# Performance work log

Hardware: AMD Instinct MI355X
Metric: run time of the kernel (lower is better)

Reference implementation:

```python
import jax, jax.numpy as jnp
import numpy as np

L_F, HOP, DELTA, L_S, COND, GH = 32, 16, 3, 96, 32, 64
B, T = 128, 48000


def setup_inputs() -> dict:
    key = jax.random.key(0)
    ks = jax.random.split(key, 12)
    s = 0.05
    return {
        "x": jax.random.normal(ks[0], (B, T), jnp.float32),
        # GRU (PyTorch layout): weight_ih (3H, L_S), weight_hh (3H, H)
        "W_ih": jax.random.normal(ks[1], (3 * GH, L_S), jnp.float32) * s,
        "W_hh": jax.random.normal(ks[2], (3 * GH, GH), jnp.float32) * s,
        "b_ih": jax.random.normal(ks[3], (3 * GH,), jnp.float32) * s,
        "b_hh": jax.random.normal(ks[4], (3 * GH,), jnp.float32) * s,
        # SlowBranch output projection -> cond_dim
        "W_cs": jax.random.normal(ks[5], (COND, GH), jnp.float32) * s,
        "b_cs": jax.random.normal(ks[6], (COND,), jnp.float32) * s,
        # FastEC MLP
        "W1": jax.random.normal(ks[7], (GH, L_F + COND), jnp.float32) * s,
        "b1": jax.random.normal(ks[8], (GH,), jnp.float32) * s,
        "W2": jax.random.normal(ks[9], (L_F, GH), jnp.float32) * s,
        "b2": jax.random.normal(ks[10], (L_F,), jnp.float32) * s,
    }


def reference(x, W_ih, W_hh, b_ih, b_hh, W_cs, b_cs, W1, b1, W2, b2):
    Bsz, Tlen = x.shape
    Nf = (Tlen - L_F) // HOP + 1
    win_s = DELTA * HOP * 2
    hop_s = DELTA * HOP
    Ns = (Tlen - win_s) // hop_s + 1

    f_starts = jnp.arange(Nf) * HOP                      # (Nf,)
    fast_idx = f_starts[:, None] + jnp.arange(L_F)       # (Nf, L_F)
    fast_frames = x[:, fast_idx]                         # (B, Nf, L_F)

    s_starts = jnp.arange(Ns) * hop_s
    slow_frames = x[:, s_starts[:, None] + jnp.arange(win_s)]  # (B, Ns, L_S)

    # Single-layer GRU over slow frames (PyTorch gate order r, z, n)
    def step(h, xt):
        gi = xt @ W_ih.T + b_ih                          # (B, 3H)
        gh = h @ W_hh.T + b_hh
        i_r, i_z, i_n = jnp.split(gi, 3, axis=-1)
        h_r, h_z, h_n = jnp.split(gh, 3, axis=-1)
        r = jax.nn.sigmoid(i_r + h_r)
        z = jax.nn.sigmoid(i_z + h_z)
        n = jnp.tanh(i_n + r * h_n)
        hn = (1.0 - z) * n + z * h
        return hn, hn

    h0 = jnp.zeros((Bsz, GH), x.dtype)
    _, hs = jax.lax.scan(step, h0, jnp.swapaxes(slow_frames, 0, 1))
    hs = jnp.swapaxes(hs, 0, 1)                          # (B, Ns, GH)
    c_s = hs @ W_cs.T + b_cs                             # (B, Ns, COND)

    # per-fast-frame conditioning vector (gather)
    idx = jnp.clip(jnp.arange(Nf) // DELTA - 1, 0, None)
    c = c_s[:, idx]                                      # (B, Nf, COND)

    # FastEC batched over all frames at once
    h = jnp.concatenate([fast_frames, c], axis=-1)       # (B, Nf, L_F+COND)
    h = jax.nn.relu(h @ W1.T + b1)
    y = h @ W2.T + b2                                    # (B, Nf, L_F)

    # overlap-add scatter
    out = jnp.zeros_like(x).at[:, fast_idx].add(y)
    return out
```

## Files before the change

kernel.cpp:

```cpp
#include <hip/hip_runtime.h>

constexpr int Bn  = 128;
constexpr int Tn  = 48000;
constexpr int NFn = 2999;
constexpr int NSn = 999;
constexpr int G3n = 192;
constexpr int GHn = 64;

typedef float f2 __attribute__((ext_vector_type(2)));
typedef float f4 __attribute__((ext_vector_type(4)));

__global__ __launch_bounds__(192) void gi_kernel(const float* __restrict__ x,
                                                 const float* __restrict__ W_ih,
                                                 const float* __restrict__ b_ih,
                                                 float* __restrict__ GI) {
  __shared__ __align__(16) float WT[48 * 196];
  __shared__ float xs[1584];
  const int tile = blockIdx.x;
  const int b    = blockIdx.y;
  const int t0   = tile * 32;
  const int nt   = min(32, NSn - t0);
  const int tid  = threadIdx.x;

  const int span = (nt - 1) * 48 + 96;
  for (int i = tid; i < 1584; i += 192)
    xs[i] = (i < span) ? x[(size_t)b * Tn + t0 * 48 + i] : 0.0f;

  const int jq = tid % 48;
  const int tg = tid / 48;
  const int j0 = jq * 4;

  float acc[8][4];
#pragma unroll
  for (int u = 0; u < 8; ++u)
#pragma unroll
    for (int jj = 0; jj < 4; ++jj) acc[u][jj] = b_ih[j0 + jj];

  for (int half = 0; half < 2; ++half) {
    __syncthreads();
    for (int e = tid; e < 192 * 48; e += 192) {
      int j = e / 48, k = e % 48;
      WT[k * 196 + j] = W_ih[j * 96 + half * 48 + k];
    }
    __syncthreads();
    for (int k = 0; k < 48; ++k) {
      float4 w = *(const float4*)&WT[k * 196 + j0];
#pragma unroll
      for (int u = 0; u < 8; ++u) {
        float xv = xs[(tg * 8 + u) * 48 + half * 48 + k];
        acc[u][0] = fmaf(xv, w.x, acc[u][0]);
        acc[u][1] = fmaf(xv, w.y, acc[u][1]);
        acc[u][2] = fmaf(xv, w.z, acc[u][2]);
        acc[u][3] = fmaf(xv, w.w, acc[u][3]);
      }
    }
  }

#pragma unroll
  for (int u = 0; u < 8; ++u) {
    int tl = tg * 8 + u;
    if (tl < nt) {
      float4 st = make_float4(acc[u][0], acc[u][1], acc[u][2], acc[u][3]);
      *(float4*)&GI[(size_t)(b * NSn + t0 + tl) * G3n + j0] = st;
    }
  }
}

__device__ __forceinline__ float fsigmoid(float v) {
  return __fdividef(1.0f, 1.0f + __expf(-v));
}
__device__ __forceinline__ float ftanh_f(float v) {
  return 1.0f - __fdividef(2.0f, __expf(2.0f * v) + 1.0f);
}

__device__ __forceinline__ void gru_body(const float* __restrict__ GI,
                                         const float* __restrict__ W_hh,
                                         const float* __restrict__ b_hh,
                                         float* __restrict__ hs,
                                         float* hbuf, int b, int j) {
  f2 wr2[32], wz2[32], wn2[32];
  const f2* Wr = (const f2*)(W_hh + (size_t)j * 64);
  const f2* Wz = (const f2*)(W_hh + (size_t)(j + 64) * 64);
  const f2* Wn = (const f2*)(W_hh + (size_t)(j + 128) * 64);
#pragma unroll
  for (int q = 0; q < 32; ++q) { wr2[q] = Wr[q]; wz2[q] = Wz[q]; wn2[q] = Wn[q]; }
#pragma unroll
  for (int q = 0; q < 32; ++q) {
    asm volatile("" : "+v"(wr2[q]));
    asm volatile("" : "+v"(wz2[q]));
    asm volatile("" : "+v"(wn2[q]));
  }
  const float br = b_hh[j], bz = b_hh[j + 64], bn = b_hh[j + 128];

  hbuf[j] = 0.0f;
  float hj = 0.0f;
  __builtin_amdgcn_wave_barrier();

  const float* gp = GI + (size_t)b * NSn * G3n;
  float* hsp = hs + (size_t)b * NSn * GHn;

  float pr0, pr1, pr2, pz0, pz1, pz2, pn0, pn1, pn2;
  pr0 = gp[0 * G3n + j];       pz0 = gp[0 * G3n + 64 + j];  pn0 = gp[0 * G3n + 128 + j];
  pr1 = gp[1 * G3n + j];       pz1 = gp[1 * G3n + 64 + j];  pn1 = gp[1 * G3n + 128 + j];

  for (int t = 0; t < NSn; ++t) {
    const size_t off = (size_t)min(t + 2, NSn - 1) * G3n;
    pr2 = gp[off + j];
    pz2 = gp[off + 64 + j];
    pn2 = gp[off + 128 + j];

    const f2* h2 = (const f2*)hbuf;
    f2 ar0 = {0.f, 0.f}, ar1 = {0.f, 0.f}, ar2 = {0.f, 0.f}, ar3 = {0.f, 0.f};
    f2 az0 = {0.f, 0.f}, az1 = {0.f, 0.f}, az2 = {0.f, 0.f}, az3 = {0.f, 0.f};
    f2 an0 = {0.f, 0.f}, an1 = {0.f, 0.f}, an2 = {0.f, 0.f}, an3 = {0.f, 0.f};
#pragma unroll
    for (int q = 0; q < 8; ++q) {
      f2 h0 = h2[q * 4 + 0], h1 = h2[q * 4 + 1], h2v = h2[q * 4 + 2], h3 = h2[q * 4 + 3];
      ar0 += wr2[q * 4 + 0] * h0; ar1 += wr2[q * 4 + 1] * h1;
      ar2 += wr2[q * 4 + 2] * h2v; ar3 += wr2[q * 4 + 3] * h3;
      az0 += wz2[q * 4 + 0] * h0; az1 += wz2[q * 4 + 1] * h1;
      az2 += wz2[q * 4 + 2] * h2v; az3 += wz2[q * 4 + 3] * h3;
      an0 += wn2[q * 4 + 0] * h0; an1 += wn2[q * 4 + 1] * h1;
      an2 += wn2[q * 4 + 2] * h2v; an3 += wn2[q * 4 + 3] * h3;
    }
    f2 sr = (ar0 + ar1) + (ar2 + ar3);
    f2 sz = (az0 + az1) + (az2 + az3);
    f2 sn = (an0 + an1) + (an2 + an3);

    float r = fsigmoid(pr0 + br + sr.x + sr.y);
    float z = fsigmoid(pz0 + bz + sz.x + sz.y);
    float n = ftanh_f(fmaf(r, bn + sn.x + sn.y, pn0));
    float hn = fmaf(z, hj - n, n);

    __builtin_amdgcn_wave_barrier();
    hbuf[j] = hn;
    __builtin_amdgcn_wave_barrier();
    hj = hn;
    hsp[(size_t)t * GHn + j] = hn;

    pr0 = pr1; pr1 = pr2;
    pz0 = pz1; pz1 = pz2;
    pn0 = pn1; pn1 = pn2;
  }
}

__global__ __attribute__((amdgpu_flat_work_group_size(64, 64),
                          amdgpu_waves_per_eu(1, 1),
                          amdgpu_num_vgpr(256)))
void gru_kernel(const float* __restrict__ GI,
                const float* __restrict__ W_hh,
                const float* __restrict__ b_hh,
                float* __restrict__ hs) {
  __shared__ __align__(16) float hbuf[64];
  gru_body(GI, W_hh, b_hh, hs, hbuf, blockIdx.x, threadIdx.x);
}

constexpr int UCHUNK = 125;
constexpr int NCH    = 24;

__global__ __attribute__((amdgpu_flat_work_group_size(64, 64),
                          amdgpu_waves_per_eu(1, 1),
                          amdgpu_num_vgpr(256)))
void fat_kernel(const float* __restrict__ GI,
                const float* __restrict__ W_hh,
                const float* __restrict__ b_hh,
                float* __restrict__ hs,
                const float* __restrict__ x,
                const float* __restrict__ W1,
                const float* __restrict__ b1,
                float* __restrict__ U) {
  __shared__ __align__(16) float hbuf[64];
  __shared__ __align__(16) float xs[UCHUNK * 16 + 16];
  const int tid = threadIdx.x;

  if (blockIdx.x < Bn) {
    gru_body(GI, W_hh, b_hh, hs, hbuf, blockIdx.x, tid);
    return;
  }

  const int ub = blockIdx.x - Bn;
  const int b  = ub / NCH;
  const int ch = ub % NCH;
  const int fA = ch * UCHUNK;
  const int fE = min(fA + UCHUNK, NFn);
  const int o  = tid;

  const int nsamp = (fE - fA - 1) * 16 + 32;
  for (int i = tid; i < nsamp; i += 64)
    xs[i] = x[(size_t)b * Tn + fA * 16 + i];

  f4 w1f[8];
#pragma unroll
  for (int i = 0; i < 8; ++i)
    w1f[i] = *(const f4*)&W1[(size_t)o * 64 + 4 * i];
  const float bo = b1[o];
  __syncthreads();

  float* Up = U + ((size_t)b * NFn) * GHn + o;
  for (int f = fA; f < fE; ++f) {
    const f4* xq = (const f4*)&xs[(f - fA) * 16];
    float a0 = bo, a1 = 0.f, a2 = 0.f, a3 = 0.f;
#pragma unroll
    for (int i = 0; i < 8; ++i) {
      f4 xv = xq[i];
      a0 = fmaf(xv[0], w1f[i][0], a0);
      a1 = fmaf(xv[1], w1f[i][1], a1);
      a2 = fmaf(xv[2], w1f[i][2], a2);
      a3 = fmaf(xv[3], w1f[i][3], a3);
    }
    Up[(size_t)f * GHn] = (a0 + a1) + (a2 + a3);
  }
}

__global__ __launch_bounds__(256) void d_kernel(const float* __restrict__ hs,
                                                const float* __restrict__ W_cs,
                                                const float* __restrict__ b_cs,
                                                const float* __restrict__ W1,
                                                float* __restrict__ d) {
  __shared__ __align__(16) float WcT[64 * 36];
  __shared__ __align__(16) float W1cT[32 * 68];
  __shared__ __align__(16) float hsl[32 * 65];
  __shared__ __align__(16) float cloc[32 * 36];
  __shared__ __align__(16) float bcs[32];
  const int tile = blockIdx.x;
  const int b    = blockIdx.y;
  const int t0   = tile * 32;
  const int nt   = min(32, NSn - t0);
  const int tid  = threadIdx.x;

  for (int e = tid; e < 32 * 64; e += 256) {
    int i = e >> 6, k = e & 63;
    WcT[k * 36 + i] = W_cs[e];
  }
  for (int e = tid; e < 64 * 32; e += 256) {
    int o = e >> 5, i = e & 31;
    W1cT[i * 68 + o] = W1[(size_t)o * 64 + 32 + i];
  }
  for (int e = tid; e < nt * 64; e += 256) {
    int t = e >> 6, k = e & 63;
    hsl[t * 65 + k] = hs[((size_t)b * NSn + t0 + t) * GHn + k];
  }
  if (tid < 32) bcs[tid] = b_cs[tid];
  __syncthreads();

  {
    const int iq = tid & 7;
    const int t  = tid >> 3;
    if (t < nt) {
      float4 acc = *(const float4*)&bcs[iq * 4];
      const float* hr = &hsl[t * 65];
#pragma unroll 4
      for (int k = 0; k < 64; ++k) {
        float hv = hr[k];
        float4 w = *(const float4*)&WcT[k * 36 + iq * 4];
        acc.x = fmaf(w.x, hv, acc.x);
        acc.y = fmaf(w.y, hv, acc.y);
        acc.z = fmaf(w.z, hv, acc.z);
        acc.w = fmaf(w.w, hv, acc.w);
      }
      *(float4*)&cloc[t * 36 + iq * 4] = acc;
    }
  }
  __syncthreads();

  for (int it = tid; it < 32 * 16; it += 256) {
    const int oq = it & 15;
    const int t  = it >> 4;
    if (t < nt) {
      float a0 = 0.f, a1 = 0.f, a2 = 0.f, a3 = 0.f;
      const float* cr = &cloc[t * 36];
#pragma unroll 4
      for (int i = 0; i < 32; ++i) {
        float cv = cr[i];
        float4 w = *(const float4*)&W1cT[i * 68 + oq * 4];
        a0 = fmaf(w.x, cv, a0);
        a1 = fmaf(w.y, cv, a1);
        a2 = fmaf(w.z, cv, a2);
        a3 = fmaf(w.w, cv, a3);
      }
      float4 st = make_float4(a0, a1, a2, a3);
      *(float4*)&d[((size_t)b * NSn + t0 + t) * GHn + oq * 4] = st;
    }
  }
}

__global__ __launch_bounds__(256) void cs_kernel(const float* __restrict__ hs,
                                                 const float* __restrict__ W_cs,
                                                 const float* __restrict__ b_cs,
                                                 float* __restrict__ cs) {
  __shared__ __align__(16) float WcT[64 * 36];
  __shared__ __align__(16) float hsl[32 * 65];
  __shared__ __align__(16) float bcs[32];
  const int tile = blockIdx.x;
  const int b    = blockIdx.y;
  const int t0   = tile * 32;
  const int nt   = min(32, NSn - t0);
  const int tid  = threadIdx.x;

  for (int e = tid; e < 32 * 64; e += 256) {
    int i = e >> 6, k = e & 63;
    WcT[k * 36 + i] = W_cs[e];
  }
  for (int e = tid; e < nt * 64; e += 256) {
    int t = e >> 6, k = e & 63;
    hsl[t * 65 + k] = hs[((size_t)b * NSn + t0 + t) * GHn + k];
  }
  if (tid < 32) bcs[tid] = b_cs[tid];
  __syncthreads();

  const int oq = tid & 7;
  const int t  = tid >> 3;
  if (t < nt) {
    float4 acc = *(const float4*)&bcs[oq * 4];
    const float* hr = &hsl[t * 65];
#pragma unroll 4
    for (int k = 0; k < 64; ++k) {
      float hv = hr[k];
      float4 w = *(const float4*)&WcT[k * 36 + oq * 4];
      acc.x = fmaf(w.x, hv, acc.x);
      acc.y = fmaf(w.y, hv, acc.y);
      acc.z = fmaf(w.z, hv, acc.z);
      acc.w = fmaf(w.w, hv, acc.w);
    }
    *(float4*)&cs[((size_t)b * NSn + t0 + t) * 32 + oq * 4] = acc;
  }
}

__global__ __launch_bounds__(256) void out2_kernel(const float* __restrict__ U,
                                                   const float* __restrict__ d,
                                                   const float* __restrict__ W2,
                                                   const float* __restrict__ b2,
                                                   float* __restrict__ out) {
  __shared__ __align__(16) float h1loc[33 * 68];
  __shared__ __align__(16) float W2T[64 * 36];
  __shared__ __align__(16) float yloc[33 * 32];
  __shared__ __align__(16) float dloc[12][68];
  __shared__ __align__(16) float bb2[32];

  const int fb  = blockIdx.x;
  const int b   = blockIdx.y;
  const int f0  = fb * 32;
  const int nf  = min(33, NFn - f0);
  const int tid = threadIdx.x;
  const int ts0 = max(f0 / 3 - 1, 0);

  for (int e = tid; e < 32 * 64; e += 256) {
    int o = e >> 6, k = e & 63;
    W2T[k * 36 + o] = W2[e];
  }
  if (tid < 32) bb2[tid] = b2[tid];
  for (int e = tid; e < 12 * 64; e += 256) {
    int ti = e >> 6, o = e & 63;
    int ts = min(ts0 + ti, NSn - 1);
    dloc[ti][o] = d[((size_t)b * NSn + ts) * GHn + o];
  }
  __syncthreads();

  for (int it = tid; it < 33 * 16; it += 256) {
    const int lf = it >> 4, oq = it & 15;
    const int f  = f0 + lf;
    f4 s = {0.f, 0.f, 0.f, 0.f};
    if (f < NFn) {
      f4 u  = *(const f4*)&U[((size_t)b * NFn + f) * GHn + oq * 4];
      const int ti = max(f / 3 - 1, 0) - ts0;
      f4 dv = *(const f4*)&dloc[ti][oq * 4];
      s = u + dv;
#pragma unroll
      for (int c = 0; c < 4; ++c) s[c] = fmaxf(s[c], 0.f);
    }
    *(f4*)&h1loc[lf * 68 + oq * 4] = s;
  }
  __syncthreads();

  for (int it = tid; it < 33 * 8; it += 256) {
    const int lf = it >> 3, oq = it & 7;
    float4 acc = *(const float4*)&bb2[oq * 4];
    const float* hr = &h1loc[lf * 68];
#pragma unroll 4
    for (int k = 0; k < 64; ++k) {
      float hv = hr[k];
      float4 w = *(const float4*)&W2T[k * 36 + oq * 4];
      acc.x = fmaf(w.x, hv, acc.x);
      acc.y = fmaf(w.y, hv, acc.y);
      acc.z = fmaf(w.z, hv, acc.z);
      acc.w = fmaf(w.w, hv, acc.w);
    }
    *(float4*)&yloc[lf * 32 + oq * 4] = acc;
  }
  __syncthreads();

  const int s0 = f0 * 16 + 16;
  const int s1 = min(s0 + 512, Tn);
  for (int s = s0 + tid; s < s1; s += 256) {
    int f1  = s >> 4;
    int o1  = s & 15;
    int lf1 = f1 - f0;
    float v = yloc[(lf1 - 1) * 32 + o1 + 16];
    if (lf1 < nf) v += yloc[lf1 * 32 + o1];
    out[(size_t)b * Tn + s] = v;
  }
  if (fb == 0 && tid < 16) out[(size_t)b * Tn + tid] = yloc[tid];
}

__global__ __launch_bounds__(256) void out_kernel(const float* __restrict__ x,
                                                  const float* __restrict__ cs,
                                                  const float* __restrict__ W1,
                                                  const float* __restrict__ b1,
                                                  const float* __restrict__ W2,
                                                  const float* __restrict__ b2,
                                                  float* __restrict__ out) {
  __shared__ __align__(16) float A[33 * 65];
  __shared__ __align__(16) float W1T[64 * 68];
  __shared__ __align__(16) float W2T[64 * 36];
  __shared__ __align__(16) float h1loc[33 * 65];
  __shared__ __align__(16) float yloc[33 * 32];
  __shared__ __align__(16) float bb1[64];
  __shared__ __align__(16) float bb2[32];

  const int fb  = blockIdx.x;
  const int b   = blockIdx.y;
  const int f0  = fb * 32;
  const int nf  = min(33, NFn - f0);
  const int tid = threadIdx.x;

  for (int e = tid; e < 64 * 64; e += 256) {
    int o = e >> 6, k = e & 63;
    W1T[k * 68 + o] = W1[e];
  }
  for (int e = tid; e < 32 * 64; e += 256) {
    int o = e >> 6, k = e & 63;
    W2T[k * 36 + o] = W2[e];
  }
  if (tid < 64) bb1[tid] = b1[tid];
  if (tid < 32) bb2[tid] = b2[tid];

  for (int e = tid; e < 33 * 32; e += 256) {
    int lf = e >> 5, k = e & 31;
    int g = (f0 + lf) * 16 + k;
    A[lf * 65 + k] = (lf < nf && g < Tn) ? x[(size_t)b * Tn + g] : 0.0f;
  }
  for (int e = tid; e < 33 * 32; e += 256) {
    int lf = e >> 5, k = e & 31;
    int ts = max((f0 + lf) / 3 - 1, 0);
    A[lf * 65 + 32 + k] = (lf < nf) ? cs[((size_t)b * NSn + ts) * 32 + k] : 0.0f;
  }
  __syncthreads();

  for (int it = tid; it < 33 * 16; it += 256) {
    int lf = it >> 4, oq = it & 15;
    float4 acc = *(const float4*)&bb1[oq * 4];
    const float* ar = &A[lf * 65];
#pragma unroll 4
    for (int k = 0; k < 64; ++k) {
      float av = ar[k];
      float4 w = *(const float4*)&W1T[k * 68 + oq * 4];
      acc.x = fmaf(w.x, av, acc.x);
      acc.y = fmaf(w.y, av, acc.y);
      acc.z = fmaf(w.z, av, acc.z);
      acc.w = fmaf(w.w, av, acc.w);
    }
    acc.x = fmaxf(acc.x, 0.0f); acc.y = fmaxf(acc.y, 0.0f);
    acc.z = fmaxf(acc.z, 0.0f); acc.w = fmaxf(acc.w, 0.0f);
    *(float4*)&h1loc[lf * 65 + oq * 4] = acc;
  }
  __syncthreads();

  for (int it = tid; it < 33 * 8; it += 256) {
    int lf = it >> 3, oq = it & 7;
    float4 acc = *(const float4*)&bb2[oq * 4];
    const float* hr = &h1loc[lf * 65];
#pragma unroll 4
    for (int k = 0; k < 64; ++k) {
      float hv = hr[k];
      float4 w = *(const float4*)&W2T[k * 36 + oq * 4];
      acc.x = fmaf(w.x, hv, acc.x);
      acc.y = fmaf(w.y, hv, acc.y);
      acc.z = fmaf(w.z, hv, acc.z);
      acc.w = fmaf(w.w, hv, acc.w);
    }
    *(float4*)&yloc[lf * 32 + oq * 4] = acc;
  }
  __syncthreads();

  const int s0 = f0 * 16 + 16;
  const int s1 = min(s0 + 512, Tn);
  for (int s = s0 + tid; s < s1; s += 256) {
    int f1  = s >> 4;
    int o1  = s & 15;
    int lf1 = f1 - f0;
    float v = yloc[(lf1 - 1) * 32 + o1 + 16];
    if (lf1 < nf) v += yloc[lf1 * 32 + o1];
    out[(size_t)b * Tn + s] = v;
  }
  if (fb == 0 && tid < 16) out[(size_t)b * Tn + tid] = yloc[tid];
}

extern "C" void kernel_launch(void* const* d_in, const int* in_sizes, int n_in,
                              void* d_out, int out_size, void* d_ws, size_t ws_size,
                              hipStream_t stream) {
  const float* x    = (const float*)d_in[0];
  const float* W_ih = (const float*)d_in[1];
  const float* W_hh = (const float*)d_in[2];
  const float* b_ih = (const float*)d_in[3];
  const float* b_hh = (const float*)d_in[4];
  const float* W_cs = (const float*)d_in[5];
  const float* b_cs = (const float*)d_in[6];
  const float* W1   = (const float*)d_in[7];
  const float* b1   = (const float*)d_in[8];
  const float* W2   = (const float*)d_in[9];
  const float* b2   = (const float*)d_in[10];
  float* out = (float*)d_out;

  const size_t giN = (size_t)Bn * NSn * G3n;
  const size_t hsN = (size_t)Bn * NSn * GHn;
  const size_t uN  = (size_t)Bn * NFn * GHn;

  float* GI = (float*)d_ws;
  float* hs = GI + giN;

  gi_kernel<<<dim3(32, Bn), 192, 0, stream>>>(x, W_ih, b_ih, GI);

  if (ws_size >= (giN + hsN + uN) * sizeof(float)) {
    float* U = hs + hsN;
    float* d = GI;
    fat_kernel<<<Bn + Bn * NCH, 64, 0, stream>>>(GI, W_hh, b_hh, hs,
                                                 x, W1, b1, U);
    d_kernel<<<dim3(32, Bn), 256, 0, stream>>>(hs, W_cs, b_cs, W1, d);
    out2_kernel<<<dim3(94, Bn), 256, 0, stream>>>(U, d, W2, b2, out);
  } else {
    float* cs = GI;
    gru_kernel<<<Bn, 64, 0, stream>>>(GI, W_hh, b_hh, hs);
    cs_kernel<<<dim3(32, Bn), 256, 0, stream>>>(hs, W_cs, b_cs, cs);
    out_kernel<<<dim3(94, Bn), 256, 0, stream>>>(x, cs, W1, b1, W2, b2, out);
  }
}
```

Before: 771.6 us.

## Fuse GI projection and GRU into a cooperative kernel with per-chunk flags

Replaces the separate GI-projection kernel and the fat kernel with one cooperative mega kernel. Worker blocks compute GI tiles in time-chunk order and publish per-(batch, chunk) readiness counters. The GRU blocks spin on those flags and start the recurrence before all of GI is ready, so the sequential GRU overlaps with the projection and the U computation. The flags live in the output buffer, which later kernels overwrite. It relies on 1024 co-resident blocks, a grid sync, and spin-waiting with memory fences.

After: 1.344 ms. 1.74x slower.

```diff
diff --git a/kernel.cpp b/kernel.cpp
--- a/kernel.cpp
+++ b/kernel.cpp
@@ -1,4 +1,7 @@
 #include <hip/hip_runtime.h>
+#include <hip/hip_cooperative_groups.h>
+
+namespace cg = cooperative_groups;
 
 constexpr int Bn  = 128;
 constexpr int Tn  = 48000;
@@ -73,11 +76,13 @@
   return 1.0f - __fdividef(2.0f, __expf(2.0f * v) + 1.0f);
 }
 
+template <bool POLL>
 __device__ __forceinline__ void gru_body(const float* __restrict__ GI,
                                          const float* __restrict__ W_hh,
                                          const float* __restrict__ b_hh,
                                          float* __restrict__ hs,
-                                         float* hbuf, int b, int j) {
+                                         float* hbuf, int b, int j,
+                                         unsigned int* flags) {
   f2 wr2[32], wz2[32], wn2[32];
   const f2* Wr = (const f2*)(W_hh + (size_t)j * 64);
   const f2* Wz = (const f2*)(W_hh + (size_t)(j + 64) * 64);
@@ -92,6 +97,18 @@
   }
   const float br = b_hh[j], bz = b_hh[j + 64], bn = b_hh[j + 128];
 
+  unsigned int* fl = POLL ? (flags + b * 32) : nullptr;
+  int cur_tc = 0;
+  if (POLL) {
+    if (j == 0) {
+      while (__hip_atomic_load(&fl[0], __ATOMIC_ACQUIRE,
+                               __HIP_MEMORY_SCOPE_AGENT) < 3u)
+        __builtin_amdgcn_s_sleep(4);
+    }
+    __builtin_amdgcn_wave_barrier();
+    __threadfence();
+  }
+
   hbuf[j] = 0.0f;
   float hj = 0.0f;
   __builtin_amdgcn_wave_barrier();
@@ -104,7 +121,21 @@
   pr1 = gp[1 * G3n + j];       pz1 = gp[1 * G3n + 64 + j];  pn1 = gp[1 * G3n + 128 + j];
 
   for (int t = 0; t < NSn; ++t) {
-    const size_t off = (size_t)min(t + 2, NSn - 1) * G3n;
+    const int tn = min(t + 2, NSn - 1);
+    if (POLL) {
+      const int tc2 = tn >> 5;
+      if (tc2 != cur_tc) {
+        if (j == 0) {
+          while (__hip_atomic_load(&fl[tc2], __ATOMIC_ACQUIRE,
+                                   __HIP_MEMORY_SCOPE_AGENT) < 3u)
+            __builtin_amdgcn_s_sleep(4);
+        }
+        __builtin_amdgcn_wave_barrier();
+        __threadfence();
+        cur_tc = tc2;
+      }
+    }
+    const size_t off = (size_t)tn * G3n;
     pr2 = gp[off + j];
     pz2 = gp[off + 64 + j];
     pn2 = gp[off + 128 + j];
@@ -152,7 +183,7 @@
                 const float* __restrict__ b_hh,
                 float* __restrict__ hs) {
   __shared__ __align__(16) float hbuf[64];
-  gru_body(GI, W_hh, b_hh, hs, hbuf, blockIdx.x, threadIdx.x);
+  gru_body<false>(GI, W_hh, b_hh, hs, hbuf, blockIdx.x, threadIdx.x, nullptr);
 }
 
 constexpr int UCHUNK = 125;
@@ -174,7 +205,7 @@
   const int tid = threadIdx.x;
 
   if (blockIdx.x < Bn) {
-    gru_body(GI, W_hh, b_hh, hs, hbuf, blockIdx.x, tid);
+    gru_body<false>(GI, W_hh, b_hh, hs, hbuf, blockIdx.x, tid, nullptr);
     return;
   }
 
@@ -209,6 +240,136 @@
       a3 = fmaf(xv[3], w1f[i][3], a3);
     }
     Up[(size_t)f * GHn] = (a0 + a1) + (a2 + a3);
+  }
+}
+
+constexpr int NWORK  = 896;
+constexpr int NBLK   = 1024;
+constexpr int GTILES = Bn * 32 * 3;
+
+__global__ __attribute__((amdgpu_flat_work_group_size(64, 64),
+                          amdgpu_waves_per_eu(1, 1),
+                          amdgpu_num_vgpr(256)))
+void mega_kernel(float* __restrict__ GI,
+                 const float* __restrict__ W_hh,
+                 const float* __restrict__ b_hh,
+                 float* __restrict__ hs,
+                 const float* __restrict__ x,
+                 const float* __restrict__ W_ih,
+                 const float* __restrict__ b_ih,
+                 const float* __restrict__ W1,
+                 const float* __restrict__ b1,
+                 float* __restrict__ U,
+                 unsigned int* __restrict__ flags) {
+  __shared__ __align__(16) float smem[3168];
+  const int tid = threadIdx.x;
+
+  for (int i = blockIdx.x * 64 + tid; i < Bn * 32; i += NBLK * 64)
+    flags[i] = 0u;
+  __threadfence();
+  cg::this_grid().sync();
+
+  if (blockIdx.x >= NWORK) {
+    gru_body<true>(GI, W_hh, b_hh, hs, smem, blockIdx.x - NWORK, tid, flags);
+    return;
+  }
+
+  float* WQ = smem;
+  float* xs = smem + 1536;
+  const int jq = tid & 15;
+  const int tg = tid >> 4;
+  const int j0 = jq * 4;
+
+  for (int tile = blockIdx.x; tile < GTILES; tile += NWORK) {
+    const int tc = tile / (Bn * 3);
+    const int rr = tile - tc * (Bn * 3);
+    const int b  = rr / 3;
+    const int g  = rr - b * 3;
+    const int nt = min(32, NSn - tc * 32);
+    const int span = (nt - 1) * 48 + 96;
+
+    __builtin_amdgcn_wave_barrier();
+    for (int i = tid; i < 1584; i += 64)
+      xs[i] = (i < span) ? x[(size_t)b * Tn + tc * 1536 + i] : 0.0f;
+
+    float acc[8][4];
+#pragma unroll
+    for (int u = 0; u < 8; ++u)
+#pragma unroll
+      for (int jj = 0; jj < 4; ++jj) acc[u][jj] = b_ih[g * 64 + j0 + jj];
+
+    for (int q = 0; q < 4; ++q) {
+      __builtin_amdgcn_wave_barrier();
+      {
+        const float* src = &W_ih[(size_t)(g * 64 + tid) * 96 + q * 24];
+#pragma unroll
+        for (int i2 = 0; i2 < 6; ++i2) {
+          f4 v = *(const f4*)&src[4 * i2];
+#pragma unroll
+          for (int c = 0; c < 4; ++c) WQ[(i2 * 4 + c) * 64 + tid] = v[c];
+        }
+      }
+      __builtin_amdgcn_wave_barrier();
+      for (int k = 0; k < 24; ++k) {
+        f4 w = *(const f4*)&WQ[k * 64 + j0];
+#pragma unroll
+        for (int u = 0; u < 8; ++u) {
+          float xv = xs[(tg * 8 + u) * 48 + q * 24 + k];
+          acc[u][0] = fmaf(xv, w[0], acc[u][0]);
+          acc[u][1] = fmaf(xv, w[1], acc[u][1]);
+          acc[u][2] = fmaf(xv, w[2], acc[u][2]);
+          acc[u][3] = fmaf(xv, w[3], acc[u][3]);
+        }
+      }
+    }
+
+#pragma unroll
+    for (int u = 0; u < 8; ++u) {
+      int tl = tg * 8 + u;
+      if (tl < nt) {
+        float4 st = make_float4(acc[u][0], acc[u][1], acc[u][2], acc[u][3]);
+        *(float4*)&GI[((size_t)(b * NSn + tc * 32 + tl)) * G3n + g * 64 + j0] = st;
+      }
+    }
+    __threadfence();
+    if (tid == 0)
+      __hip_atomic_fetch_add(&flags[b * 32 + tc], 1u, __ATOMIC_RELEASE,
+                             __HIP_MEMORY_SCOPE_AGENT);
+  }
+
+  float* xu = smem;
+  f4 w1f[8];
+#pragma unroll
+  for (int i = 0; i < 8; ++i)
+    w1f[i] = *(const f4*)&W1[(size_t)tid * 64 + 4 * i];
+  const float bo = b1[tid];
+
+  for (int ut = blockIdx.x; ut < Bn * NCH; ut += NWORK) {
+    const int b  = ut / NCH;
+    const int ch = ut % NCH;
+    const int fA = ch * UCHUNK;
+    const int fE = min(fA + UCHUNK, NFn);
+    const int nsamp = (fE - fA - 1) * 16 + 32;
+
+    __builtin_amdgcn_wave_barrier();
+    for (int i = tid; i < nsamp; i += 64)
+      xu[i] = x[(size_t)b * Tn + fA * 16 + i];
+    __builtin_amdgcn_wave_barrier();
+
+    float* Up = U + ((size_t)b * NFn) * GHn + tid;
+    for (int f = fA; f < fE; ++f) {
+      const f4* xq = (const f4*)&xu[(f - fA) * 16];
+      float a0 = bo, a1 = 0.f, a2 = 0.f, a3 = 0.f;
+#pragma unroll
+      for (int i = 0; i < 8; ++i) {
+        f4 xv = xq[i];
+        a0 = fmaf(xv[0], w1f[i][0], a0);
+        a1 = fmaf(xv[1], w1f[i][1], a1);
+        a2 = fmaf(xv[2], w1f[i][2], a2);
+        a3 = fmaf(xv[3], w1f[i][3], a3);
+      }
+      Up[(size_t)f * GHn] = (a0 + a1) + (a2 + a3);
+    }
   }
 }
 
@@ -518,17 +679,28 @@
   float* GI = (float*)d_ws;
   float* hs = GI + giN;
 
-  gi_kernel<<<dim3(32, Bn), 192, 0, stream>>>(x, W_ih, b_ih, GI);
-
   if (ws_size >= (giN + hsN + uN) * sizeof(float)) {
     float* U = hs + hsN;
     float* d = GI;
-    fat_kernel<<<Bn + Bn * NCH, 64, 0, stream>>>(GI, W_hh, b_hh, hs,
-                                                 x, W1, b1, U);
+    unsigned int* flags = (unsigned int*)out;
+
+    void* args[] = {(void*)&GI, (void*)&W_hh, (void*)&b_hh, (void*)&hs,
+                    (void*)&x,  (void*)&W_ih, (void*)&b_ih, (void*)&W1,
+                    (void*)&b1, (void*)&U,    (void*)&flags};
+    hipError_t e = hipLaunchCooperativeKernel((const void*)mega_kernel,
+                                              dim3(NBLK), dim3(64),
+                                              args, 0, stream);
+    if (e != hipSuccess) {
+      (void)hipGetLastError();
+      gi_kernel<<<dim3(32, Bn), 192, 0, stream>>>(x, W_ih, b_ih, GI);
+      fat_kernel<<<Bn + Bn * NCH, 64, 0, stream>>>(GI, W_hh, b_hh, hs,
+                                                   x, W1, b1, U);
+    }
     d_kernel<<<dim3(32, Bn), 256, 0, stream>>>(hs, W_cs, b_cs, W1, d);
     out2_kernel<<<dim3(94, Bn), 256, 0, stream>>>(U, d, W2, b2, out);
   } else {
     float* cs = GI;
+    gi_kernel<<<dim3(32, Bn), 192, 0, stream>>>(x, W_ih, b_ih, GI);
     gru_kernel<<<Bn, 64, 0, stream>>>(GI, W_hh, b_hh, hs);
     cs_kernel<<<dim3(32, Bn), 256, 0, stream>>>(hs, W_cs, b_cs, cs);
     out_kernel<<<dim3(94, Bn), 256, 0, stream>>>(x, cs, W1, b1, W2, b2, out);
```

## Rewrite GI projection kernel to keep W_ih row in registers per thread

Applied to the files above, without the earlier changes.

Replaces the shared-memory tiled GI kernel with one where each thread holds its full 96-wide W_ih row in registers and streams x frames directly from global memory, two timesteps at a time. Each thread produces one output column across a chunk of 56 slow frames, and the grid shrinks to 18 chunks per batch row. This removes the shared x staging and the transposed weight tile, in exchange for high register pressure (96 weight floats) and redundant broadcast global loads of x across threads. GI is only a small part of the pipeline, so the end-to-end effect is limited.

Result: slower. 870.1 us (+12.8%).

```diff
diff --git a/kernel.cpp b/kernel.cpp
--- a/kernel.cpp
+++ b/kernel.cpp
@@ -10,59 +10,69 @@
 typedef float f2 __attribute__((ext_vector_type(2)));
 typedef float f4 __attribute__((ext_vector_type(4)));
 
-__global__ __launch_bounds__(192) void gi_kernel(const float* __restrict__ x,
-                                                 const float* __restrict__ W_ih,
-                                                 const float* __restrict__ b_ih,
-                                                 float* __restrict__ GI) {
-  __shared__ __align__(16) float WT[48 * 196];
-  __shared__ float xs[1584];
-  const int tile = blockIdx.x;
-  const int b    = blockIdx.y;
-  const int t0   = tile * 32;
-  const int nt   = min(32, NSn - t0);
-  const int tid  = threadIdx.x;
-
-  const int span = (nt - 1) * 48 + 96;
-  for (int i = tid; i < 1584; i += 192)
-    xs[i] = (i < span) ? x[(size_t)b * Tn + t0 * 48 + i] : 0.0f;
-
-  const int jq = tid % 48;
-  const int tg = tid / 48;
-  const int j0 = jq * 4;
-
-  float acc[8][4];
-#pragma unroll
-  for (int u = 0; u < 8; ++u)
-#pragma unroll
-    for (int jj = 0; jj < 4; ++jj) acc[u][jj] = b_ih[j0 + jj];
-
-  for (int half = 0; half < 2; ++half) {
+constexpr int GI_TC = 56;
+constexpr int GI_NC = 18;
+
+__global__ __launch_bounds__(192) void gi2_kernel(const float* __restrict__ x,
+                                                  const float* __restrict__ W_ih,
+                                                  const float* __restrict__ b_ih,
+                                                  float* __restrict__ GI) {
+  __shared__ __align__(16) float WL[192 * 48];
+  const int b  = blockIdx.y;
+  const int t0 = blockIdx.x * GI_TC;
+  const int t1 = min(t0 + GI_TC, NSn);
+  const int j  = threadIdx.x;
+
+  f4 w[24];
+  for (int h = 0; h < 2; ++h) {
     __syncthreads();
-    for (int e = tid; e < 192 * 48; e += 192) {
-      int j = e / 48, k = e % 48;
-      WT[k * 196 + j] = W_ih[j * 96 + half * 48 + k];
+    for (int e = j; e < 192 * 48; e += 192) {
+      const int row = e / 48, kk = e - row * 48;
+      WL[e] = W_ih[row * 96 + h * 48 + kk];
     }
     __syncthreads();
-    for (int k = 0; k < 48; ++k) {
-      float4 w = *(const float4*)&WT[k * 196 + j0];
-#pragma unroll
-      for (int u = 0; u < 8; ++u) {
-        float xv = xs[(tg * 8 + u) * 48 + half * 48 + k];
-        acc[u][0] = fmaf(xv, w.x, acc[u][0]);
-        acc[u][1] = fmaf(xv, w.y, acc[u][1]);
-        acc[u][2] = fmaf(xv, w.z, acc[u][2]);
-        acc[u][3] = fmaf(xv, w.w, acc[u][3]);
-      }
-    }
-  }
-
-#pragma unroll
-  for (int u = 0; u < 8; ++u) {
-    int tl = tg * 8 + u;
-    if (tl < nt) {
-      float4 st = make_float4(acc[u][0], acc[u][1], acc[u][2], acc[u][3]);
-      *(float4*)&GI[(size_t)(b * NSn + t0 + tl) * G3n + j0] = st;
-    }
+#pragma unroll
+    for (int i = 0; i < 12; ++i)
+      w[h * 12 + i] = *(const f4*)&WL[j * 48 + 4 * i];
+  }
+  const float bj = b_ih[j];
+
+  const float* xb = x + (size_t)b * Tn;
+  float* gbase = GI + (size_t)b * NSn * G3n + j;
+
+  int t = t0;
+  for (; t + 2 <= t1; t += 2) {
+    const float* xp0 = xb + t * 48;
+    const float* xp1 = xp0 + 48;
+    float a0 = bj, a1 = bj;
+#pragma unroll
+    for (int q = 0; q < 24; ++q) {
+      f4 x0 = *(const f4*)&xp0[4 * q];
+      f4 x1 = *(const f4*)&xp1[4 * q];
+      a0 = fmaf(x0[0], w[q][0], a0);
+      a0 = fmaf(x0[1], w[q][1], a0);
+      a0 = fmaf(x0[2], w[q][2], a0);
+      a0 = fmaf(x0[3], w[q][3], a0);
+      a1 = fmaf(x1[0], w[q][0], a1);
+      a1 = fmaf(x1[1], w[q][1], a1);
+      a1 = fmaf(x1[2], w[q][2], a1);
+      a1 = fmaf(x1[3], w[q][3], a1);
+    }
+    gbase[(size_t)t * G3n]       = a0;
+    gbase[(size_t)(t + 1) * G3n] = a1;
+  }
+  for (; t < t1; ++t) {
+    const float* xp = xb + t * 48;
+    float a0 = bj;
+#pragma unroll
+    for (int q = 0; q < 24; ++q) {
+      f4 xv = *(const f4*)&xp[4 * q];
+      a0 = fmaf(xv[0], w[q][0], a0);
+      a0 = fmaf(xv[1], w[q][1], a0);
+      a0 = fmaf(xv[2], w[q][2], a0);
+      a0 = fmaf(xv[3], w[q][3], a0);
+    }
+    gbase[(size_t)t * G3n] = a0;
   }
 }
 
@@ -518,7 +528,7 @@
   float* GI = (float*)d_ws;
   float* hs = GI + giN;
 
-  gi_kernel<<<dim3(32, Bn), 192, 0, stream>>>(x, W_ih, b_ih, GI);
+  gi2_kernel<<<dim3(GI_NC, Bn), 192, 0, stream>>>(x, W_ih, b_ih, GI);
 
   if (ws_size >= (giN + hsN + uN) * sizeof(float)) {
     float* U = hs + hsN;
```
